# Kernel optimization log

Measured on AMD Instinct MI355X. Metric: run time of the kernel, lower is better.

The kernel has to match this reference:

```python
import jax, jax.numpy as jnp
import numpy as np

TOP_K = 2

def setup_inputs() -> dict:
    key = jax.random.key(0)
    k0, k1, k2 = jax.random.split(key, 3)
    N, D, E = 32768, 1024, 8  # tokens, in_dim, expert_num
    x = jax.random.normal(k0, (N, D), dtype=jnp.float32)
    W1 = jax.random.normal(k1, (D // 2, D), dtype=jnp.float32) * (1.0 / np.sqrt(D))
    b1 = jnp.zeros((D // 2,), dtype=jnp.float32)
    W2 = jax.random.normal(k2, (E, D // 2), dtype=jnp.float32) * (1.0 / np.sqrt(D // 2))
    b2 = jnp.zeros((E,), dtype=jnp.float32)
    return {"x": x, "W1": W1, "b1": b1, "W2": W2, "b2": b2}

def reference(x, W1, b1, W2, b2):
    E = W2.shape[0]
    # gate: two stacked Linears (no nonlinearity between, as in source)
    h = x @ W1.T + b1                      # [N, D/2]
    router_logits = h @ W2.T + b2          # [N, E]
    router_probs = jax.nn.softmax(router_logits, axis=-1)
    router_weights, top_k_indices = jax.lax.top_k(router_probs, TOP_K)  # [N, K]
    router_weights = router_weights / jnp.sum(router_weights, axis=-1, keepdims=True)
    expert_masks = jax.nn.one_hot(top_k_indices, E, dtype=jnp.int32)   # [N, K, E]
    expert_masks = jnp.transpose(expert_masks, (2, 1, 0))              # [E, K, N]
    return (router_logits, router_weights, top_k_indices, expert_masks)
```

## Files before the change

### kernel.cpp

```cpp
#include <hip/hip_runtime.h>
#include <math.h>


#define N_TOK 32768
#define D_IN  1024
#define D_H   512
#define N_EXP 8

#define BM      128
#define BK      16
#define THREADS 512
#define NKT     (D_IN / BK)
#define WSLOTS  (NKT * 1024)

typedef _Float16 f16;
typedef __attribute__((ext_vector_type(4)))  _Float16 f16x4;
typedef __attribute__((ext_vector_type(8)))  _Float16 f16x8;
typedef __attribute__((ext_vector_type(16))) float    f32x16;

#define MFMA(a, b, c) __builtin_amdgcn_mfma_f32_32x32x16_f16((a), (b), (c), 0, 0, 0)

#define GLOAD16(gsrc, ldst)                                                    \
    __builtin_amdgcn_global_load_lds(                                          \
        (const __attribute__((address_space(1))) void*)(gsrc),                 \
        (__attribute__((address_space(3))) void*)(ldst), 16, 0, 0)

__global__ void split_w1(const float* __restrict__ W1,
                         f16* __restrict__ wsH, f16* __restrict__ wsL) {
    const int s = blockIdx.x * 256 + threadIdx.x;
    const int kt  = s >> 10;
    const int ctg = (s >> 6) & 15;
    const int l   = s & 63;
    const int n   = ctg * 32 + (l & 31);
    const int k   = kt * BK + (l >> 5) * 8;
    const float* src = &W1[(size_t)n * D_IN + k];
    float4 a0 = *(const float4*)src;
    float4 a1 = *(const float4*)(src + 4);
    f16x8 hi, lo;
#pragma unroll
    for (int j = 0; j < 4; ++j) {
        float v0 = ((const float*)&a0)[j];
        float v1 = ((const float*)&a1)[j];
        _Float16 h0 = (_Float16)v0, h1 = (_Float16)v1;
        hi[j] = h0;     hi[j + 4] = h1;
        lo[j] = (_Float16)(v0 - (float)h0);
        lo[j + 4] = (_Float16)(v1 - (float)h1);
    }
    *(f16x8*)&wsH[(size_t)s * 8] = hi;
    *(f16x8*)&wsL[(size_t)s * 8] = lo;
}

__global__ __launch_bounds__(THREADS, 1)
void moe_router_mfma(const float* __restrict__ x,
                     const f16* __restrict__ wH,
                     const f16* __restrict__ wL,
                     const float* __restrict__ b1,
                     const float* __restrict__ W2,
                     const float* __restrict__ b2,
                     float* __restrict__ out)
{
    __shared__ __align__(16) f16 AS[2 * 2 * 2048];
    __shared__ __align__(16) unsigned char BB[65536];
    __shared__ __align__(16) float W2s[N_EXP * D_H];
    __shared__ __align__(16) float b1s[D_H];
    __shared__ float b2s[N_EXP];

    const int t    = threadIdx.x;
    const int w    = t >> 6;
    const int lane = t & 63;
    const int m0   = blockIdx.x * BM;

    f32x16 a0c0 = {}, a0c1 = {}, a1c0 = {}, a1c1 = {};
    f32x16 a2c0 = {}, a2c1 = {}, a3c0 = {}, a3c1 = {};

    const int fA   = t >> 1;
    const int qA   = t & 1;
    const int rowA = (fA >> 6) * 32 + (fA & 31);
    const int kA   = ((fA >> 5) & 1) * 8 + qA * 4;
    const float* xsrc = x + (size_t)(m0 + rowA) * D_IN + kA;
    const int aOff = t * 8;
    const int aDst = fA * 8 + qA * 4;
    (void)aOff;

    auto stageB = [&](int kt, int buf) {
        const size_t base = (size_t)kt * 8192;
        f16* bh = (f16*)(BB + buf * 32768);
        f16* bl = (f16*)(BB + buf * 32768 + 16384);
        GLOAD16(wH + base + (size_t)t * 8,         bh + w * 512);
        GLOAD16(wH + base + (size_t)(512 + t) * 8, bh + 4096 + w * 512);
        GLOAD16(wL + base + (size_t)t * 8,         bl + w * 512);
        GLOAD16(wL + base + (size_t)(512 + t) * 8, bl + 4096 + w * 512);
    };
    auto stageAwrite = [&](const float4& xv, int buf) {
        f16x4 hi, lo;
        float v[4] = {xv.x, xv.y, xv.z, xv.w};
#pragma unroll
        for (int j = 0; j < 4; ++j) {
            _Float16 h = (_Float16)v[j];
            hi[j] = h;
            lo[j] = (_Float16)(v[j] - (float)h);
        }
        *(f16x4*)&AS[(buf * 2 + 0) * 2048 + aDst] = hi;
        *(f16x4*)&AS[(buf * 2 + 1) * 2048 + aDst] = lo;
    };

    {
        float4 xv = *(const float4*)xsrc;
        stageB(0, 0);
        stageAwrite(xv, 0);
    }
    __syncthreads();

    for (int kt = 0; kt < NKT; ++kt) {
        const int cur = kt & 1;
        const int nxt = cur ^ 1;

        float4 xv;
        if (kt + 1 < NKT) {
            xv = *(const float4*)(xsrc + (size_t)(kt + 1) * BK);
            stageB(kt + 1, nxt);
        }

        const f16* ah = &AS[(cur * 2 + 0) * 2048];
        const f16* al = &AS[(cur * 2 + 1) * 2048];
        const f16* bh = (const f16*)(BB + cur * 32768);
        const f16* bl = (const f16*)(BB + cur * 32768 + 16384);

        f16x8 ah0 = *(const f16x8*)&ah[(0 * 64 + lane) * 8];
        f16x8 ah1 = *(const f16x8*)&ah[(1 * 64 + lane) * 8];
        f16x8 ah2 = *(const f16x8*)&ah[(2 * 64 + lane) * 8];
        f16x8 ah3 = *(const f16x8*)&ah[(3 * 64 + lane) * 8];
        f16x8 al0 = *(const f16x8*)&al[(0 * 64 + lane) * 8];
        f16x8 al1 = *(const f16x8*)&al[(1 * 64 + lane) * 8];
        f16x8 al2 = *(const f16x8*)&al[(2 * 64 + lane) * 8];
        f16x8 al3 = *(const f16x8*)&al[(3 * 64 + lane) * 8];
        f16x8 bh0 = *(const f16x8*)&bh[((2 * w + 0) * 64 + lane) * 8];
        f16x8 bh1 = *(const f16x8*)&bh[((2 * w + 1) * 64 + lane) * 8];
        f16x8 bl0 = *(const f16x8*)&bl[((2 * w + 0) * 64 + lane) * 8];
        f16x8 bl1 = *(const f16x8*)&bl[((2 * w + 1) * 64 + lane) * 8];

        a0c0 = MFMA(ah0, bh0, a0c0); a0c0 = MFMA(al0, bh0, a0c0); a0c0 = MFMA(ah0, bl0, a0c0);
        a1c0 = MFMA(ah1, bh0, a1c0); a1c0 = MFMA(al1, bh0, a1c0); a1c0 = MFMA(ah1, bl0, a1c0);
        a2c0 = MFMA(ah2, bh0, a2c0); a2c0 = MFMA(al2, bh0, a2c0); a2c0 = MFMA(ah2, bl0, a2c0);
        a3c0 = MFMA(ah3, bh0, a3c0); a3c0 = MFMA(al3, bh0, a3c0); a3c0 = MFMA(ah3, bl0, a3c0);
        a0c1 = MFMA(ah0, bh1, a0c1); a0c1 = MFMA(al0, bh1, a0c1); a0c1 = MFMA(ah0, bl1, a0c1);
        a1c1 = MFMA(ah1, bh1, a1c1); a1c1 = MFMA(al1, bh1, a1c1); a1c1 = MFMA(ah1, bl1, a1c1);
        a2c1 = MFMA(ah2, bh1, a2c1); a2c1 = MFMA(al2, bh1, a2c1); a2c1 = MFMA(ah2, bl1, a2c1);
        a3c1 = MFMA(ah3, bh1, a3c1); a3c1 = MFMA(al3, bh1, a3c1); a3c1 = MFMA(ah3, bl1, a3c1);

        if (kt + 1 < NKT) stageAwrite(xv, nxt);

        __syncthreads();
    }

    ((float4*)W2s)[t * 2]     = ((const float4*)W2)[t * 2];
    ((float4*)W2s)[t * 2 + 1] = ((const float4*)W2)[t * 2 + 1];
    if (t < D_H / 4) ((float4*)b1s)[t] = ((const float4*)b1)[t];
    if (t < N_EXP) b2s[t] = b2[t];
    __syncthreads();

    const int n0  = w * 64 + (lane & 31);
    const int n1  = n0 + 32;
    const float bn0 = b1s[n0];
    const float bn1 = b1s[n1];
    float* h_s = (float*)BB;

    float* out_logits = out;
    float* out_w      = out + (size_t)N_TOK * N_EXP;
    float* out_i      = out_w + (size_t)N_TOK * 2;
    float* out_m      = out_i + (size_t)N_TOK * 2;

    auto reduce_rows = [&](int rt) {
#pragma unroll
        for (int rr2 = 0; rr2 < 4; ++rr2) {
            const int rl   = w * 4 + rr2;
            const int grow = m0 + rt * 32 + rl;
            float4 ha = *(const float4*)&h_s[rl * 512 + lane * 4];
            float4 hb = *(const float4*)&h_s[rl * 512 + 256 + lane * 4];
            float v1 = -3.4e38f, v2 = -3.4e38f;
            int   i1 = 0, i2 = 0;
            float pls[8];
#pragma unroll
            for (int e = 0; e < N_EXP; ++e) {
                float4 wa = *(const float4*)&W2s[e * D_H + lane * 4];
                float4 wb = *(const float4*)&W2s[e * D_H + 256 + lane * 4];
                float s = ha.x * wa.x;
                s = fmaf(ha.y, wa.y, s);
                s = fmaf(ha.z, wa.z, s);
                s = fmaf(ha.w, wa.w, s);
                s = fmaf(hb.x, wb.x, s);
                s = fmaf(hb.y, wb.y, s);
                s = fmaf(hb.z, wb.z, s);
                s = fmaf(hb.w, wb.w, s);
#pragma unroll
                for (int off = 1; off < 64; off <<= 1)
                    s += __shfl_xor(s, off);
                s += b2s[e];
                pls[e] = s;
                if (s > v1)      { v2 = v1; i2 = i1; v1 = s; i1 = e; }
                else if (s > v2) { v2 = s;  i2 = e; }
            }
            const float rr   = expf(v2 - v1);
            const float wden = 1.f / (1.f + rr);
            if (lane == 0) {
                float4 lo4 = {pls[0], pls[1], pls[2], pls[3]};
                float4 hi4 = {pls[4], pls[5], pls[6], pls[7]};
                *(float4*)&out_logits[(size_t)grow * N_EXP]     = lo4;
                *(float4*)&out_logits[(size_t)grow * N_EXP + 4] = hi4;
                float2 wv = {wden, rr * wden};
                *(float2*)&out_w[(size_t)grow * 2] = wv;
                float2 iv = {(float)i1, (float)i2};
                *(float2*)&out_i[(size_t)grow * 2] = iv;
            }
            if (lane < 16) {
                const int e   = lane >> 1;
                const int kk  = lane & 1;
                const int sel = kk ? i2 : i1;
                out_m[((size_t)(e * 2 + kk)) * N_TOK + grow] = (sel == e) ? 1.0f : 0.0f;
            }
        }
    };

#define DO_GROUP(AC0, AC1, RT) do {                                            \
        _Pragma("unroll")                                                      \
        for (int rr = 0; rr < 16; ++rr) {                                      \
            const int rl = (rr & 3) + 8 * (rr >> 2) + 4 * (lane >> 5);         \
            h_s[rl * 512 + n0] = AC0[rr] + bn0;                                \
            h_s[rl * 512 + n1] = AC1[rr] + bn1;                                \
        }                                                                      \
        __syncthreads();                                                       \
        reduce_rows(RT);                                                       \
        __syncthreads();                                                       \
    } while (0)

    DO_GROUP(a0c0, a0c1, 0);
    DO_GROUP(a1c0, a1c1, 1);
    DO_GROUP(a2c0, a2c1, 2);
    DO_GROUP(a3c0, a3c1, 3);
#undef DO_GROUP
}

extern "C" void kernel_launch(void* const* d_in, const int* in_sizes, int n_in,
                              void* d_out, int out_size, void* d_ws, size_t ws_size,
                              hipStream_t stream) {
    const float* x  = (const float*)d_in[0];
    const float* W1 = (const float*)d_in[1];
    const float* b1 = (const float*)d_in[2];
    const float* W2 = (const float*)d_in[3];
    const float* b2 = (const float*)d_in[4];
    float* out = (float*)d_out;

    f16* wsH = (f16*)d_ws;
    f16* wsL = wsH + (size_t)WSLOTS * 8;

    split_w1<<<WSLOTS / 256, 256, 0, stream>>>(W1, wsH, wsL);
    moe_router_mfma<<<N_TOK / BM, THREADS, 0, stream>>>(x, wsH, wsL, b1, W2, b2, out);
}
```

Measured before the change: 141.3 us.

## Load W1 fragments directly into registers instead of staging through LDS

Each wave now reads its W1 hi/lo MFMA fragments straight from global memory into registers, double-buffered across an unrolled pair of iterations, instead of async-copying them into shared memory. This removes the 64KB LDS B buffer and the LDS reads for B, since each wave only uses its own B slice. It also adds s_setprio around MFMA groups and a mid-iteration s_barrier to stagger waves. The risks are exposed global-load latency without LDS staging and more register pressure from the extra fragment buffers.

After: 130.6 us. -7.6%, faster.

```diff
diff --git a/kernel.cpp b/kernel.cpp
--- a/kernel.cpp
+++ b/kernel.cpp
@@ -19,11 +19,6 @@
 typedef __attribute__((ext_vector_type(16))) float    f32x16;
 
 #define MFMA(a, b, c) __builtin_amdgcn_mfma_f32_32x32x16_f16((a), (b), (c), 0, 0, 0)
-
-#define GLOAD16(gsrc, ldst)                                                    \
-    __builtin_amdgcn_global_load_lds(                                          \
-        (const __attribute__((address_space(1))) void*)(gsrc),                 \
-        (__attribute__((address_space(3))) void*)(ldst), 16, 0, 0)
 
 __global__ void split_w1(const float* __restrict__ W1,
                          f16* __restrict__ wsH, f16* __restrict__ wsL) {
@@ -59,8 +54,8 @@
                      const float* __restrict__ b2,
                      float* __restrict__ out)
 {
-    __shared__ __align__(16) f16 AS[2 * 2 * 2048];
-    __shared__ __align__(16) unsigned char BB[65536];
+    __shared__ __align__(16) f16   AS[2 * 2 * 2048];
+    __shared__ __align__(16) float h_s[32 * 512];
     __shared__ __align__(16) float W2s[N_EXP * D_H];
     __shared__ __align__(16) float b1s[D_H];
     __shared__ float b2s[N_EXP];
@@ -78,19 +73,11 @@
     const int rowA = (fA >> 6) * 32 + (fA & 31);
     const int kA   = ((fA >> 5) & 1) * 8 + qA * 4;
     const float* xsrc = x + (size_t)(m0 + rowA) * D_IN + kA;
-    const int aOff = t * 8;
     const int aDst = fA * 8 + qA * 4;
-    (void)aOff;
-
-    auto stageB = [&](int kt, int buf) {
-        const size_t base = (size_t)kt * 8192;
-        f16* bh = (f16*)(BB + buf * 32768);
-        f16* bl = (f16*)(BB + buf * 32768 + 16384);
-        GLOAD16(wH + base + (size_t)t * 8,         bh + w * 512);
-        GLOAD16(wH + base + (size_t)(512 + t) * 8, bh + 4096 + w * 512);
-        GLOAD16(wL + base + (size_t)t * 8,         bl + w * 512);
-        GLOAD16(wL + base + (size_t)(512 + t) * 8, bl + 4096 + w * 512);
-    };
+
+    const size_t bOff0 = (size_t)(2 * w + 0) * 512 + (size_t)lane * 8;
+    const size_t bOff1 = (size_t)(2 * w + 1) * 512 + (size_t)lane * 8;
+
     auto stageAwrite = [&](const float4& xv, int buf) {
         f16x4 hi, lo;
         float v[4] = {xv.x, xv.y, xv.z, xv.w};
@@ -104,54 +91,67 @@
         *(f16x4*)&AS[(buf * 2 + 1) * 2048 + aDst] = lo;
     };
 
+    f16x8 Bh0A = *(const f16x8*)(wH + bOff0);
+    f16x8 Bh1A = *(const f16x8*)(wH + bOff1);
+    f16x8 Bl0A = *(const f16x8*)(wL + bOff0);
+    f16x8 Bl1A = *(const f16x8*)(wL + bOff1);
+    f16x8 Bh0B, Bh1B, Bl0B, Bl1B;
     {
         float4 xv = *(const float4*)xsrc;
-        stageB(0, 0);
         stageAwrite(xv, 0);
     }
     __syncthreads();
 
-    for (int kt = 0; kt < NKT; ++kt) {
-        const int cur = kt & 1;
-        const int nxt = cur ^ 1;
-
-        float4 xv;
-        if (kt + 1 < NKT) {
-            xv = *(const float4*)(xsrc + (size_t)(kt + 1) * BK);
-            stageB(kt + 1, nxt);
-        }
-
-        const f16* ah = &AS[(cur * 2 + 0) * 2048];
-        const f16* al = &AS[(cur * 2 + 1) * 2048];
-        const f16* bh = (const f16*)(BB + cur * 32768);
-        const f16* bl = (const f16*)(BB + cur * 32768 + 16384);
-
-        f16x8 ah0 = *(const f16x8*)&ah[(0 * 64 + lane) * 8];
-        f16x8 ah1 = *(const f16x8*)&ah[(1 * 64 + lane) * 8];
-        f16x8 ah2 = *(const f16x8*)&ah[(2 * 64 + lane) * 8];
-        f16x8 ah3 = *(const f16x8*)&ah[(3 * 64 + lane) * 8];
-        f16x8 al0 = *(const f16x8*)&al[(0 * 64 + lane) * 8];
-        f16x8 al1 = *(const f16x8*)&al[(1 * 64 + lane) * 8];
-        f16x8 al2 = *(const f16x8*)&al[(2 * 64 + lane) * 8];
-        f16x8 al3 = *(const f16x8*)&al[(3 * 64 + lane) * 8];
-        f16x8 bh0 = *(const f16x8*)&bh[((2 * w + 0) * 64 + lane) * 8];
-        f16x8 bh1 = *(const f16x8*)&bh[((2 * w + 1) * 64 + lane) * 8];
-        f16x8 bl0 = *(const f16x8*)&bl[((2 * w + 0) * 64 + lane) * 8];
-        f16x8 bl1 = *(const f16x8*)&bl[((2 * w + 1) * 64 + lane) * 8];
-
-        a0c0 = MFMA(ah0, bh0, a0c0); a0c0 = MFMA(al0, bh0, a0c0); a0c0 = MFMA(ah0, bl0, a0c0);
-        a1c0 = MFMA(ah1, bh0, a1c0); a1c0 = MFMA(al1, bh0, a1c0); a1c0 = MFMA(ah1, bl0, a1c0);
-        a2c0 = MFMA(ah2, bh0, a2c0); a2c0 = MFMA(al2, bh0, a2c0); a2c0 = MFMA(ah2, bl0, a2c0);
-        a3c0 = MFMA(ah3, bh0, a3c0); a3c0 = MFMA(al3, bh0, a3c0); a3c0 = MFMA(ah3, bl0, a3c0);
-        a0c1 = MFMA(ah0, bh1, a0c1); a0c1 = MFMA(al0, bh1, a0c1); a0c1 = MFMA(ah0, bl1, a0c1);
-        a1c1 = MFMA(ah1, bh1, a1c1); a1c1 = MFMA(al1, bh1, a1c1); a1c1 = MFMA(ah1, bl1, a1c1);
-        a2c1 = MFMA(ah2, bh1, a2c1); a2c1 = MFMA(al2, bh1, a2c1); a2c1 = MFMA(ah2, bl1, a2c1);
-        a3c1 = MFMA(ah3, bh1, a3c1); a3c1 = MFMA(al3, bh1, a3c1); a3c1 = MFMA(ah3, bl1, a3c1);
-
-        if (kt + 1 < NKT) stageAwrite(xv, nxt);
-
-        __syncthreads();
+#define BODY(BUF, KT, BH0, BH1, BL0, BL1, NH0, NH1, NL0, NL1) do {             \
+        float4 xnxt = {0.f, 0.f, 0.f, 0.f};                                    \
+        if ((KT) + 1 < NKT) {                                                  \
+            const size_t nb = (size_t)((KT) + 1) * 8192;                       \
+            NH0 = *(const f16x8*)(wH + nb + bOff0);                            \
+            NH1 = *(const f16x8*)(wH + nb + bOff1);                            \
+            NL0 = *(const f16x8*)(wL + nb + bOff0);                            \
+            NL1 = *(const f16x8*)(wL + nb + bOff1);                            \
+            xnxt = *(const float4*)(xsrc + (size_t)((KT) + 1) * BK);           \
+        }                                                                      \
+        const f16* ah = &AS[((BUF) * 2 + 0) * 2048];                           \
+        const f16* al = &AS[((BUF) * 2 + 1) * 2048];                           \
+        f16x8 ah0 = *(const f16x8*)&ah[(0 * 64 + lane) * 8];                   \
+        f16x8 al0 = *(const f16x8*)&al[(0 * 64 + lane) * 8];                   \
+        f16x8 ah1 = *(const f16x8*)&ah[(1 * 64 + lane) * 8];                   \
+        f16x8 al1 = *(const f16x8*)&al[(1 * 64 + lane) * 8];                   \
+        f16x8 ah2 = *(const f16x8*)&ah[(2 * 64 + lane) * 8];                   \
+        f16x8 al2 = *(const f16x8*)&al[(2 * 64 + lane) * 8];                   \
+        f16x8 ah3 = *(const f16x8*)&ah[(3 * 64 + lane) * 8];                   \
+        f16x8 al3 = *(const f16x8*)&al[(3 * 64 + lane) * 8];                   \
+        __builtin_amdgcn_s_setprio(1);                                         \
+        a0c0 = MFMA(ah0, BH0, a0c0); a0c0 = MFMA(al0, BH0, a0c0);              \
+        a0c0 = MFMA(ah0, BL0, a0c0);                                           \
+        a1c0 = MFMA(ah1, BH0, a1c0); a1c0 = MFMA(al1, BH0, a1c0);              \
+        a1c0 = MFMA(ah1, BL0, a1c0);                                           \
+        a2c0 = MFMA(ah2, BH0, a2c0); a2c0 = MFMA(al2, BH0, a2c0);              \
+        a2c0 = MFMA(ah2, BL0, a2c0);                                           \
+        a3c0 = MFMA(ah3, BH0, a3c0); a3c0 = MFMA(al3, BH0, a3c0);              \
+        a3c0 = MFMA(ah3, BL0, a3c0);                                           \
+        __builtin_amdgcn_s_setprio(0);                                         \
+        __builtin_amdgcn_s_barrier();                                          \
+        __builtin_amdgcn_s_setprio(1);                                         \
+        a0c1 = MFMA(ah0, BH1, a0c1); a0c1 = MFMA(al0, BH1, a0c1);              \
+        a0c1 = MFMA(ah0, BL1, a0c1);                                           \
+        a1c1 = MFMA(ah1, BH1, a1c1); a1c1 = MFMA(al1, BH1, a1c1);              \
+        a1c1 = MFMA(ah1, BL1, a1c1);                                           \
+        a2c1 = MFMA(ah2, BH1, a2c1); a2c1 = MFMA(al2, BH1, a2c1);              \
+        a2c1 = MFMA(ah2, BL1, a2c1);                                           \
+        a3c1 = MFMA(ah3, BH1, a3c1); a3c1 = MFMA(al3, BH1, a3c1);              \
+        a3c1 = MFMA(ah3, BL1, a3c1);                                           \
+        __builtin_amdgcn_s_setprio(0);                                         \
+        if ((KT) + 1 < NKT) stageAwrite(xnxt, (BUF) ^ 1);                      \
+        __syncthreads();                                                       \
+    } while (0)
+
+    for (int kt = 0; kt < NKT; kt += 2) {
+        BODY(0, kt,     Bh0A, Bh1A, Bl0A, Bl1A, Bh0B, Bh1B, Bl0B, Bl1B);
+        BODY(1, kt + 1, Bh0B, Bh1B, Bl0B, Bl1B, Bh0A, Bh1A, Bl0A, Bl1A);
     }
+#undef BODY
 
     ((float4*)W2s)[t * 2]     = ((const float4*)W2)[t * 2];
     ((float4*)W2s)[t * 2 + 1] = ((const float4*)W2)[t * 2 + 1];
@@ -163,7 +163,6 @@
     const int n1  = n0 + 32;
     const float bn0 = b1s[n0];
     const float bn1 = b1s[n1];
-    float* h_s = (float*)BB;
 
     float* out_logits = out;
     float* out_w      = out + (size_t)N_TOK * N_EXP;
```

## Load W1 fragments directly from global into registers and double K-step per barrier

Applied to the files above, without the earlier changes.

Removes the LDS staging of the pre-split W1 hi/lo operands (global_load_lds) and instead has each wave load its B fragments straight from global memory into registers, since each wave uses a disjoint slice. The K loop now processes two 16-wide K tiles per iteration, halving barrier count, and wraps MFMA blocks with s_setprio to favour matrix issue. This trades LDS traffic and sync for per-iteration global-load latency that is no longer prefetched a stage ahead, relying on the L2 cache and wave overlap to hide it.

After: 133.0 us. -5.9%, faster.

```diff
diff --git a/kernel.cpp b/kernel.cpp
--- a/kernel.cpp
+++ b/kernel.cpp
@@ -8,10 +8,9 @@
 #define N_EXP 8
 
 #define BM      128
-#define BK      16
 #define THREADS 512
-#define NKT     (D_IN / BK)
-#define WSLOTS  (NKT * 1024)
+#define NKT2    32
+#define WSLOTS  (64 * 1024)
 
 typedef _Float16 f16;
 typedef __attribute__((ext_vector_type(4)))  _Float16 f16x4;
@@ -19,11 +18,6 @@
 typedef __attribute__((ext_vector_type(16))) float    f32x16;
 
 #define MFMA(a, b, c) __builtin_amdgcn_mfma_f32_32x32x16_f16((a), (b), (c), 0, 0, 0)
-
-#define GLOAD16(gsrc, ldst)                                                    \
-    __builtin_amdgcn_global_load_lds(                                          \
-        (const __attribute__((address_space(1))) void*)(gsrc),                 \
-        (__attribute__((address_space(3))) void*)(ldst), 16, 0, 0)
 
 __global__ void split_w1(const float* __restrict__ W1,
                          f16* __restrict__ wsH, f16* __restrict__ wsL) {
@@ -32,7 +26,7 @@
     const int ctg = (s >> 6) & 15;
     const int l   = s & 63;
     const int n   = ctg * 32 + (l & 31);
-    const int k   = kt * BK + (l >> 5) * 8;
+    const int k   = kt * 16 + (l >> 5) * 8;
     const float* src = &W1[(size_t)n * D_IN + k];
     float4 a0 = *(const float4*)src;
     float4 a1 = *(const float4*)(src + 4);
@@ -59,11 +53,13 @@
                      const float* __restrict__ b2,
                      float* __restrict__ out)
 {
-    __shared__ __align__(16) f16 AS[2 * 2 * 2048];
-    __shared__ __align__(16) unsigned char BB[65536];
+    __shared__ __align__(16) unsigned char SMEM[65536];
     __shared__ __align__(16) float W2s[N_EXP * D_H];
     __shared__ __align__(16) float b1s[D_H];
     __shared__ float b2s[N_EXP];
+
+    f16*   AS  = (f16*)SMEM;
+    float* h_s = (float*)SMEM;
 
     const int t    = threadIdx.x;
     const int w    = t >> 6;
@@ -78,20 +74,12 @@
     const int rowA = (fA >> 6) * 32 + (fA & 31);
     const int kA   = ((fA >> 5) & 1) * 8 + qA * 4;
     const float* xsrc = x + (size_t)(m0 + rowA) * D_IN + kA;
-    const int aOff = t * 8;
     const int aDst = fA * 8 + qA * 4;
-    (void)aOff;
-
-    auto stageB = [&](int kt, int buf) {
-        const size_t base = (size_t)kt * 8192;
-        f16* bh = (f16*)(BB + buf * 32768);
-        f16* bl = (f16*)(BB + buf * 32768 + 16384);
-        GLOAD16(wH + base + (size_t)t * 8,         bh + w * 512);
-        GLOAD16(wH + base + (size_t)(512 + t) * 8, bh + 4096 + w * 512);
-        GLOAD16(wL + base + (size_t)t * 8,         bl + w * 512);
-        GLOAD16(wL + base + (size_t)(512 + t) * 8, bl + 4096 + w * 512);
-    };
-    auto stageAwrite = [&](const float4& xv, int buf) {
+
+    const size_t bOff0 = (size_t)(2 * w + 0) * 512 + (size_t)lane * 8;
+    const size_t bOff1 = (size_t)(2 * w + 1) * 512 + (size_t)lane * 8;
+
+    auto stageAwrite = [&](const float4& xv, int buf, int sub) {
         f16x4 hi, lo;
         float v[4] = {xv.x, xv.y, xv.z, xv.w};
 #pragma unroll
@@ -100,56 +88,86 @@
             hi[j] = h;
             lo[j] = (_Float16)(v[j] - (float)h);
         }
-        *(f16x4*)&AS[(buf * 2 + 0) * 2048 + aDst] = hi;
-        *(f16x4*)&AS[(buf * 2 + 1) * 2048 + aDst] = lo;
+        *(f16x4*)&AS[(buf * 2 + 0) * 4096 + sub * 2048 + aDst] = hi;
+        *(f16x4*)&AS[(buf * 2 + 1) * 4096 + sub * 2048 + aDst] = lo;
     };
 
     {
-        float4 xv = *(const float4*)xsrc;
-        stageB(0, 0);
-        stageAwrite(xv, 0);
+        float4 xv0 = *(const float4*)xsrc;
+        float4 xv1 = *(const float4*)(xsrc + 16);
+        stageAwrite(xv0, 0, 0);
+        stageAwrite(xv1, 0, 1);
     }
     __syncthreads();
 
-    for (int kt = 0; kt < NKT; ++kt) {
-        const int cur = kt & 1;
+    for (int ktt = 0; ktt < NKT2; ++ktt) {
+        const int cur = ktt & 1;
         const int nxt = cur ^ 1;
-
-        float4 xv;
-        if (kt + 1 < NKT) {
-            xv = *(const float4*)(xsrc + (size_t)(kt + 1) * BK);
-            stageB(kt + 1, nxt);
-        }
-
-        const f16* ah = &AS[(cur * 2 + 0) * 2048];
-        const f16* al = &AS[(cur * 2 + 1) * 2048];
-        const f16* bh = (const f16*)(BB + cur * 32768);
-        const f16* bl = (const f16*)(BB + cur * 32768 + 16384);
-
-        f16x8 ah0 = *(const f16x8*)&ah[(0 * 64 + lane) * 8];
-        f16x8 ah1 = *(const f16x8*)&ah[(1 * 64 + lane) * 8];
-        f16x8 ah2 = *(const f16x8*)&ah[(2 * 64 + lane) * 8];
-        f16x8 ah3 = *(const f16x8*)&ah[(3 * 64 + lane) * 8];
-        f16x8 al0 = *(const f16x8*)&al[(0 * 64 + lane) * 8];
-        f16x8 al1 = *(const f16x8*)&al[(1 * 64 + lane) * 8];
-        f16x8 al2 = *(const f16x8*)&al[(2 * 64 + lane) * 8];
-        f16x8 al3 = *(const f16x8*)&al[(3 * 64 + lane) * 8];
-        f16x8 bh0 = *(const f16x8*)&bh[((2 * w + 0) * 64 + lane) * 8];
-        f16x8 bh1 = *(const f16x8*)&bh[((2 * w + 1) * 64 + lane) * 8];
-        f16x8 bl0 = *(const f16x8*)&bl[((2 * w + 0) * 64 + lane) * 8];
-        f16x8 bl1 = *(const f16x8*)&bl[((2 * w + 1) * 64 + lane) * 8];
-
-        a0c0 = MFMA(ah0, bh0, a0c0); a0c0 = MFMA(al0, bh0, a0c0); a0c0 = MFMA(ah0, bl0, a0c0);
-        a1c0 = MFMA(ah1, bh0, a1c0); a1c0 = MFMA(al1, bh0, a1c0); a1c0 = MFMA(ah1, bl0, a1c0);
-        a2c0 = MFMA(ah2, bh0, a2c0); a2c0 = MFMA(al2, bh0, a2c0); a2c0 = MFMA(ah2, bl0, a2c0);
-        a3c0 = MFMA(ah3, bh0, a3c0); a3c0 = MFMA(al3, bh0, a3c0); a3c0 = MFMA(ah3, bl0, a3c0);
-        a0c1 = MFMA(ah0, bh1, a0c1); a0c1 = MFMA(al0, bh1, a0c1); a0c1 = MFMA(ah0, bl1, a0c1);
-        a1c1 = MFMA(ah1, bh1, a1c1); a1c1 = MFMA(al1, bh1, a1c1); a1c1 = MFMA(ah1, bl1, a1c1);
-        a2c1 = MFMA(ah2, bh1, a2c1); a2c1 = MFMA(al2, bh1, a2c1); a2c1 = MFMA(ah2, bl1, a2c1);
-        a3c1 = MFMA(ah3, bh1, a3c1); a3c1 = MFMA(al3, bh1, a3c1); a3c1 = MFMA(ah3, bl1, a3c1);
-
-        if (kt + 1 < NKT) stageAwrite(xv, nxt);
-
+        const size_t kb0 = (size_t)(2 * ktt) * 8192;
+        const size_t kb1 = (size_t)(2 * ktt + 1) * 8192;
+
+        f16x8 B0h0 = *(const f16x8*)(wH + kb0 + bOff0);
+        f16x8 B0h1 = *(const f16x8*)(wH + kb0 + bOff1);
+        f16x8 B0l0 = *(const f16x8*)(wL + kb0 + bOff0);
+        f16x8 B0l1 = *(const f16x8*)(wL + kb0 + bOff1);
+        f16x8 B1h0 = *(const f16x8*)(wH + kb1 + bOff0);
+        f16x8 B1h1 = *(const f16x8*)(wH + kb1 + bOff1);
+        f16x8 B1l0 = *(const f16x8*)(wL + kb1 + bOff0);
+        f16x8 B1l1 = *(const f16x8*)(wL + kb1 + bOff1);
+        float4 xn0 = {0.f, 0.f, 0.f, 0.f}, xn1 = {0.f, 0.f, 0.f, 0.f};
+        if (ktt + 1 < NKT2) {
+            xn0 = *(const float4*)(xsrc + (size_t)(ktt + 1) * 32);
+            xn1 = *(const float4*)(xsrc + (size_t)(ktt + 1) * 32 + 16);
+        }
+
+        const f16* ah = &AS[(cur * 2 + 0) * 4096];
+        const f16* al = &AS[(cur * 2 + 1) * 4096];
+
+        {
+            f16x8 ah0 = *(const f16x8*)&ah[(0 * 64 + lane) * 8];
+            f16x8 al0 = *(const f16x8*)&al[(0 * 64 + lane) * 8];
+            f16x8 ah1 = *(const f16x8*)&ah[(1 * 64 + lane) * 8];
+            f16x8 al1 = *(const f16x8*)&al[(1 * 64 + lane) * 8];
+            f16x8 ah2 = *(const f16x8*)&ah[(2 * 64 + lane) * 8];
+            f16x8 al2 = *(const f16x8*)&al[(2 * 64 + lane) * 8];
+            f16x8 ah3 = *(const f16x8*)&ah[(3 * 64 + lane) * 8];
+            f16x8 al3 = *(const f16x8*)&al[(3 * 64 + lane) * 8];
+            __builtin_amdgcn_s_setprio(1);
+            a0c0 = MFMA(ah0, B0h0, a0c0); a0c0 = MFMA(al0, B0h0, a0c0); a0c0 = MFMA(ah0, B0l0, a0c0);
+            a1c0 = MFMA(ah1, B0h0, a1c0); a1c0 = MFMA(al1, B0h0, a1c0); a1c0 = MFMA(ah1, B0l0, a1c0);
+            a2c0 = MFMA(ah2, B0h0, a2c0); a2c0 = MFMA(al2, B0h0, a2c0); a2c0 = MFMA(ah2, B0l0, a2c0);
+            a3c0 = MFMA(ah3, B0h0, a3c0); a3c0 = MFMA(al3, B0h0, a3c0); a3c0 = MFMA(ah3, B0l0, a3c0);
+            a0c1 = MFMA(ah0, B0h1, a0c1); a0c1 = MFMA(al0, B0h1, a0c1); a0c1 = MFMA(ah0, B0l1, a0c1);
+            a1c1 = MFMA(ah1, B0h1, a1c1); a1c1 = MFMA(al1, B0h1, a1c1); a1c1 = MFMA(ah1, B0l1, a1c1);
+            a2c1 = MFMA(ah2, B0h1, a2c1); a2c1 = MFMA(al2, B0h1, a2c1); a2c1 = MFMA(ah2, B0l1, a2c1);
+            a3c1 = MFMA(ah3, B0h1, a3c1); a3c1 = MFMA(al3, B0h1, a3c1); a3c1 = MFMA(ah3, B0l1, a3c1);
+            __builtin_amdgcn_s_setprio(0);
+        }
+        {
+            f16x8 ah0 = *(const f16x8*)&ah[2048 + (0 * 64 + lane) * 8];
+            f16x8 al0 = *(const f16x8*)&al[2048 + (0 * 64 + lane) * 8];
+            f16x8 ah1 = *(const f16x8*)&ah[2048 + (1 * 64 + lane) * 8];
+            f16x8 al1 = *(const f16x8*)&al[2048 + (1 * 64 + lane) * 8];
+            f16x8 ah2 = *(const f16x8*)&ah[2048 + (2 * 64 + lane) * 8];
+            f16x8 al2 = *(const f16x8*)&al[2048 + (2 * 64 + lane) * 8];
+            f16x8 ah3 = *(const f16x8*)&ah[2048 + (3 * 64 + lane) * 8];
+            f16x8 al3 = *(const f16x8*)&al[2048 + (3 * 64 + lane) * 8];
+            __builtin_amdgcn_s_setprio(1);
+            a0c0 = MFMA(ah0, B1h0, a0c0); a0c0 = MFMA(al0, B1h0, a0c0); a0c0 = MFMA(ah0, B1l0, a0c0);
+            a1c0 = MFMA(ah1, B1h0, a1c0); a1c0 = MFMA(al1, B1h0, a1c0); a1c0 = MFMA(ah1, B1l0, a1c0);
+            a2c0 = MFMA(ah2, B1h0, a2c0); a2c0 = MFMA(al2, B1h0, a2c0); a2c0 = MFMA(ah2, B1l0, a2c0);
+            a3c0 = MFMA(ah3, B1h0, a3c0); a3c0 = MFMA(al3, B1h0, a3c0); a3c0 = MFMA(ah3, B1l0, a3c0);
+            a0c1 = MFMA(ah0, B1h1, a0c1); a0c1 = MFMA(al0, B1h1, a0c1); a0c1 = MFMA(ah0, B1l1, a0c1);
+            a1c1 = MFMA(ah1, B1h1, a1c1); a1c1 = MFMA(al1, B1h1, a1c1); a1c1 = MFMA(ah1, B1l1, a1c1);
+            a2c1 = MFMA(ah2, B1h1, a2c1); a2c1 = MFMA(al2, B1h1, a2c1); a2c1 = MFMA(ah2, B1l1, a2c1);
+            a3c1 = MFMA(ah3, B1h1, a3c1); a3c1 = MFMA(al3, B1h1, a3c1); a3c1 = MFMA(ah3, B1l1, a3c1);
+            __builtin_amdgcn_s_setprio(0);
+        }
+
+        if (ktt + 1 < NKT2) {
+            stageAwrite(xn0, nxt, 0);
+            stageAwrite(xn1, nxt, 1);
+        }
         __syncthreads();
     }
 
@@ -163,7 +181,6 @@
     const int n1  = n0 + 32;
     const float bn0 = b1s[n0];
     const float bn1 = b1s[n1];
-    float* h_s = (float*)BB;
 
     float* out_logits = out;
     float* out_w      = out + (size_t)N_TOK * N_EXP;
```
